# Optimization experiments

Measured on AMD Instinct MI355X. Metric: run time of the kernel, lower is better.

The kernel has to match this reference:

```python
import jax, jax.numpy as jnp
import numpy as np
from jax import lax

SIZE = 64
N_SUPPORT = 8192
N_QUERIES = 16384
UNROLLING_STEPS = 10


def setup_inputs() -> dict:
    key = jax.random.key(0)
    ks = jax.random.split(key, 6)
    s = 1.0 / np.sqrt(SIZE)
    return {
        "support": jax.random.normal(ks[0], (N_SUPPORT, SIZE), jnp.float32),
        "queries": jax.random.normal(ks[1], (N_QUERIES, SIZE), jnp.float32),
        "W_ih": jax.random.normal(ks[2], (4 * SIZE, SIZE), jnp.float32) * s,
        "W_hh": jax.random.normal(ks[3], (4 * SIZE, SIZE), jnp.float32) * s,
        "b_ih": jax.random.normal(ks[4], (4 * SIZE,), jnp.float32) * s,
        "b_hh": jax.random.normal(ks[5], (4 * SIZE,), jnp.float32) * s,
    }


def _lstm_cell(x, h, c, W_ih, W_hh, b_ih, b_hh):
    # PyTorch LSTMCell gate order: i, f, g, o
    gates = x @ W_ih.T + b_ih + h @ W_hh.T + b_hh  # [B, 4*size]
    i, f, g, o = jnp.split(gates, 4, axis=1)
    c_new = jax.nn.sigmoid(f) * c + jax.nn.sigmoid(i) * jnp.tanh(g)
    h_new = jax.nn.sigmoid(o) * jnp.tanh(c_new)
    return h_new, c_new


def reference(support, queries, W_ih, W_hh, b_ih, b_hh):
    def step(carry, _):
        h_hat, c = carry
        h = h_hat + queries                              # [B, size]
        att = jax.nn.softmax(h @ support.T, axis=1)      # [B, n_support]
        readout = att @ support                          # [B, size]
        h_hat2, c2 = _lstm_cell(queries, h + readout, c, W_ih, W_hh, b_ih, b_hh)
        return (h_hat2, c2), None

    init = (jnp.zeros_like(queries), jnp.zeros_like(queries))
    (h_hat, _), _ = lax.scan(step, init, None, length=UNROLLING_STEPS)
    return h_hat + queries
```

## Files before the change

kernel.cpp:

```cpp
#include <hip/hip_runtime.h>

using u16 = unsigned short;
using u32 = unsigned int;

#define NS 8192
#define NQ 16384
#define SZ 64
#define STEPS 10
#define TS 64
#define TSZ (TS * SZ)
#define NT (NS / TS)
#define NR (NT / 2)
#define L2E 1.44269504088896340736f

typedef __attribute__((ext_vector_type(8))) _Float16 f16x8;
typedef __attribute__((ext_vector_type(4))) float f32x4;

static __device__ __forceinline__ float ex2(float x) { float r; asm("v_exp_f32 %0, %1" : "=v"(r) : "v"(x)); return r; }
static __device__ __forceinline__ float rcp_(float x) { float r; asm("v_rcp_f32 %0, %1" : "=v"(r) : "v"(x)); return r; }

static __device__ __forceinline__ u16 hbits(_Float16 h) { union { _Float16 h; u16 u; } c; c.h = h; return c.u; }
static __device__ __forceinline__ u32 pk2(float lo, float hi) {
    return (u32)hbits((_Float16)lo) | ((u32)hbits((_Float16)hi) << 16);
}
static __device__ __forceinline__ f32x4 MMH(f16x8 a, f16x8 b, f32x4 c) {
    return __builtin_amdgcn_mfma_f32_16x16x32_f16(a, b, c, 0, 0, 0);
}
static __device__ __forceinline__ f16x8 LD(const void* p) { return *(const f16x8*)p; }
static __device__ __forceinline__ float sig(float x) { return rcp_(1.f + ex2(-L2E * x)); }
static __device__ __forceinline__ float tanh_(float x) {
    float e = ex2(-2.f * L2E * x);
    return (1.f - e) * rcp_(1.f + e);
}
static __device__ __forceinline__ void lds_fence() {
    asm volatile("s_waitcnt lgkmcnt(0)" ::: "memory");
    __builtin_amdgcn_sched_barrier(0);
}
static __device__ __forceinline__ void gload16(const void* g, void* l) {
    __builtin_amdgcn_global_load_lds(
        (const __attribute__((address_space(1))) void*)g,
        (__attribute__((address_space(3))) void*)l, 16, 0, 0);
}

__global__ void prep_kernel(const float* __restrict__ sup,
                            const float* __restrict__ Wih,
                            const float* __restrict__ Whh,
                            const float* __restrict__ bih,
                            const float* __restrict__ bhh,
                            u16* __restrict__ supH, u16* __restrict__ supL,
                            u16* __restrict__ supT,
                            u16* __restrict__ WiH, u16* __restrict__ WiL,
                            u16* __restrict__ WhH, u16* __restrict__ WhL,
                            float* __restrict__ bs) {
    int i = blockIdx.x * 256 + threadIdx.x;
    if (i < NS * SZ) {
        float v = sup[i];
        _Float16 hi = (_Float16)v;
        _Float16 lo = (_Float16)(v - (float)hi);
        supH[i] = hbits(hi);
        supL[i] = hbits(lo);
        int s = i >> 6, d = i & 63;
        supT[(s >> 6) * TSZ + d * TS + (s & 63)] = hbits(hi);
    }
    if (i < 4 * SZ * SZ) {
        float a = Wih[i]; _Float16 ah = (_Float16)a;
        WiH[i] = hbits(ah); WiL[i] = hbits((_Float16)(a - (float)ah));
        float b = Whh[i]; _Float16 bh = (_Float16)b;
        WhH[i] = hbits(bh); WhL[i] = hbits((_Float16)(b - (float)bh));
    }
    if (i < 4 * SZ) bs[i] = bih[i] + bhh[i];
}

__global__ __launch_bounds__(1024) void attlstm_kernel(
    const float* __restrict__ queries,
    const u16* __restrict__ supH, const u16* __restrict__ supL,
    const u16* __restrict__ supT,
    const u16* __restrict__ WiH, const u16* __restrict__ WiL,
    const u16* __restrict__ WhH, const u16* __restrict__ WhL,
    const float* __restrict__ bsum,
    float* __restrict__ out) {
    __shared__ __align__(16) u16 stage[4][3][TSZ];
    __shared__ __align__(16) u32 P_lds[16][512];
    __shared__ __align__(16) u16 hsl[4][2048];
    __shared__ __align__(16) float bs_lds[256];

    const int tid = threadIdx.x;
    const int w = tid >> 6;
    const int l = tid & 63;
    const int qg = w & 3;
    const int quarter = w >> 2;
    const int tsel = quarter >> 1;
    const int shalf = quarter & 1;
    const int q = l & 15;
    const int g = l >> 4;
    const int qrow = blockIdx.x * 64 + qg * 16 + q;
    const u32 swz = (u32)(q & 7) << 4;
    const u32 bsl = (u32)q * 128 + ((32u * (u32)quarter + 8u * (u32)g) ^ swz);

    if (tid < 256) bs_lds[tid] = bsum[tid];

    const u16* gsrc[3]; int inoff[3]; int ctsel[3];
#pragma unroll
    for (int j = 0; j < 3; ++j) {
        int c = w + 16 * j;
        ctsel[j] = c / 24;
        int rem = c - 24 * ctsel[j];
        int a = rem >> 3, s8 = rem & 7;
        int srcoff = (s8 * 8 + (l >> 3)) * SZ + ((l & 7) ^ (l >> 3)) * 8;
        gsrc[j] = ((a == 0) ? supH : (a == 1) ? supL : supT) + srcoff;
        inoff[j] = a * TSZ + s8 * 512;
    }
    u16* stg = &stage[0][0][0];
    char* hslb = (char*)&hsl[qg][0];
    char* pw = (char*)&P_lds[w][0];

    float qv[4], hh[4], cc[4];
    {
        f32x4 v = *(const f32x4*)&queries[qrow * SZ + 16 * quarter + 4 * g];
#pragma unroll
        for (int jj = 0; jj < 4; ++jj) { qv[jj] = v[jj]; hh[jj] = 0.f; cc[jj] = 0.f; }
        _Float16 c0 = (_Float16)v[0], c1 = (_Float16)v[1], c2 = (_Float16)v[2], c3 = (_Float16)v[3];
        uint2 whi, wlo;
        whi.x = (u32)hbits(c0) | ((u32)hbits(c1) << 16);
        whi.y = (u32)hbits(c2) | ((u32)hbits(c3) << 16);
        wlo.x = pk2(v[0] - (float)c0, v[1] - (float)c1);
        wlo.y = pk2(v[2] - (float)c2, v[3] - (float)c3);
        *(uint2*)(hslb + bsl) = whi;
        *(uint2*)(hslb + 2048 + bsl) = wlo;
    }
    __syncthreads();
    const f16x8 qfh0 = LD(hslb + q * 128 + ((16u * g) ^ swz));
    const f16x8 qfh1 = LD(hslb + q * 128 + ((16u * g + 64u) ^ swz));
    const f16x8 qfl0 = LD(hslb + 2048 + q * 128 + ((16u * g) ^ swz));
    const f16x8 qfl1 = LD(hslb + 2048 + q * 128 + ((16u * g + 64u) ^ swz));

#pragma unroll 1
    for (int step = 0; step < STEPS; ++step) {
        __syncthreads();
        {
            float h0 = hh[0] + qv[0], h1 = hh[1] + qv[1], h2 = hh[2] + qv[2], h3 = hh[3] + qv[3];
            _Float16 a0 = (_Float16)h0, a1 = (_Float16)h1, a2 = (_Float16)h2, a3 = (_Float16)h3;
            uint2 whi, wlo;
            whi.x = (u32)hbits(a0) | ((u32)hbits(a1) << 16);
            whi.y = (u32)hbits(a2) | ((u32)hbits(a3) << 16);
            wlo.x = pk2(h0 - (float)a0, h1 - (float)a1);
            wlo.y = pk2(h2 - (float)a2, h3 - (float)a3);
            *(uint2*)(hslb + bsl) = whi;
            *(uint2*)(hslb + 2048 + bsl) = wlo;
        }
        __syncthreads();
        const f16x8 bh0 = LD(hslb + q * 128 + ((16u * g) ^ swz));
        const f16x8 bh1 = LD(hslb + q * 128 + ((16u * g + 64u) ^ swz));
        const f16x8 bl0 = LD(hslb + 2048 + q * 128 + ((16u * g) ^ swz));
        const f16x8 bl1 = LD(hslb + 2048 + q * 128 + ((16u * g + 64u) ^ swz));

#pragma unroll
        for (int j = 0; j < 3; ++j)
            gload16(gsrc[j] + ctsel[j] * TSZ, stg + ctsel[j] * 12288 + inoff[j]);
        __syncthreads();

        float m = -1e30f, mL = -1.5e30f, lsum = 0.f;
        f32x4 Oa[4] = {{0, 0, 0, 0}, {0, 0, 0, 0}, {0, 0, 0, 0}, {0, 0, 0, 0}};

#pragma unroll 1
        for (int r = 0; r < NR; ++r) {
            if (r < NR - 1) {
#pragma unroll
                for (int j = 0; j < 3; ++j) {
                    int t = 2 * r + 2 + ctsel[j];
                    gload16(gsrc[j] + t * TSZ, stg + (t & 3) * 12288 + inoff[j]);
                }
            }
            const int myslot = (2 * r + tsel) & 3;
            const char* sH = (const char*)(stg + myslot * 12288);
            const char* sL = sH + TSZ * 2;
            const char* sT = sH + 2 * TSZ * 2;
            f32x4 sv[2];
#pragma unroll
            for (int sub = 0; sub < 2; ++sub) {
                u32 rb = (u32)(16 * (2 * shalf + sub) + q) * 128;
                f16x8 aH0 = LD(sH + rb + ((16u * g) ^ swz));
                f16x8 aH1 = LD(sH + rb + ((16u * g + 64u) ^ swz));
                f16x8 aL0 = LD(sL + rb + ((16u * g) ^ swz));
                f16x8 aL1 = LD(sL + rb + ((16u * g + 64u) ^ swz));
                f32x4 a = {0, 0, 0, 0};
                a = MMH(aH0, bh0, a); a = MMH(aH1, bh1, a);
                a = MMH(aH0, bl0, a); a = MMH(aH1, bl1, a);
                a = MMH(aL0, bh0, a); a = MMH(aL1, bh1, a);
                sv[sub] = a;
            }
            float tm = fmaxf(fmaxf(fmaxf(sv[0][0], sv[0][1]), fmaxf(sv[0][2], sv[0][3])),
                             fmaxf(fmaxf(sv[1][0], sv[1][1]), fmaxf(sv[1][2], sv[1][3])));
            tm = fmaxf(tm, __shfl_xor(tm, 16));
            tm = fmaxf(tm, __shfl_xor(tm, 32));
            if (__any(tm > m + 5.5f)) {
                float mn = fmaxf(m, tm);
                float sc = ex2((m - mn) * L2E);
                lsum *= sc;
                Oa[0] *= sc; Oa[1] *= sc; Oa[2] *= sc; Oa[3] *= sc;
                m = mn; mL = m * L2E;
            }
#pragma unroll
            for (int sub = 0; sub < 2; ++sub) {
                float p0 = ex2(sv[sub][0] * L2E - mL);
                float p1 = ex2(sv[sub][1] * L2E - mL);
                float p2 = ex2(sv[sub][2] * L2E - mL);
                float p3 = ex2(sv[sub][3] * L2E - mL);
                lsum += (p0 + p1) + (p2 + p3);
                uint2 wv; wv.x = pk2(p0, p1); wv.y = pk2(p2, p3);
                *(uint2*)(pw + q * 128 + ((32u * sub + 8u * g) ^ swz)) = wv;
            }
            lds_fence();
            f16x8 pb = LD(pw + q * 128 + ((16u * g) ^ swz));
            u32 kbT = (16u * g + 64u * shalf) ^ swz;
#pragma unroll
            for (int dsub = 0; dsub < 4; ++dsub) {
                f16x8 aT = LD(sT + (u32)(16 * dsub + q) * 128 + kbT);
                Oa[dsub] = MMH(aT, pb, Oa[dsub]);
            }
            __syncthreads();
        }
        lsum += __shfl_xor(lsum, 16);
        lsum += __shfl_xor(lsum, 32);

        float* mg = (float*)stg;
        float* mine = mg + (u32)(w * 64 + l) * 20;
        *(f32x4*)(mine + 0) = Oa[0];
        *(f32x4*)(mine + 4) = Oa[1];
        *(f32x4*)(mine + 8) = Oa[2];
        *(f32x4*)(mine + 12) = Oa[3];
        mine[16] = m; mine[17] = lsum;
        __syncthreads();

        float mk[4], lk[4];
        f32x4 Ok[4];
#pragma unroll
        for (int k = 0; k < 4; ++k) {
            const float* oth = mg + (u32)((qg + 4 * k) * 64 + l) * 20;
            Ok[k] = *(const f32x4*)(oth + 4 * quarter);
            mk[k] = oth[16]; lk[k] = oth[17];
        }
        float M = fmaxf(fmaxf(mk[0], mk[1]), fmaxf(mk[2], mk[3]));
        f32x4 Op = {0, 0, 0, 0};
        float ls = 0.f;
#pragma unroll
        for (int k = 0; k < 4; ++k) {
            float sk = ex2((mk[k] - M) * L2E);
            ls += lk[k] * sk;
            Op += Ok[k] * sk;
        }
        float inv = rcp_(ls);

        {
            float r0 = hh[0] + qv[0] + Op[0] * inv;
            float r1 = hh[1] + qv[1] + Op[1] * inv;
            float r2 = hh[2] + qv[2] + Op[2] * inv;
            float r3 = hh[3] + qv[3] + Op[3] * inv;
            _Float16 a0 = (_Float16)r0, a1 = (_Float16)r1, a2 = (_Float16)r2, a3 = (_Float16)r3;
            uint2 whi, wlo;
            whi.x = (u32)hbits(a0) | ((u32)hbits(a1) << 16);
            whi.y = (u32)hbits(a2) | ((u32)hbits(a3) << 16);
            wlo.x = pk2(r0 - (float)a0, r1 - (float)a1);
            wlo.y = pk2(r2 - (float)a2, r3 - (float)a3);
            *(uint2*)(hslb + bsl) = whi;
            *(uint2*)(hslb + 2048 + bsl) = wlo;
        }
        __syncthreads();
        const f16x8 rh0 = LD(hslb + q * 128 + ((16u * g) ^ swz));
        const f16x8 rh1 = LD(hslb + q * 128 + ((16u * g + 64u) ^ swz));
        const f16x8 rl0 = LD(hslb + 2048 + q * 128 + ((16u * g) ^ swz));
        const f16x8 rl1 = LD(hslb + 2048 + q * 128 + ((16u * g + 64u) ^ swz));

        f32x4 ga[4];
#pragma unroll
        for (int ch = 0; ch < 4; ++ch) {
            int u_ = 4 * ch + quarter;
            f32x4 a = *(const f32x4*)&bs_lds[16 * u_ + 4 * g];
            const u16* wiH = WiH + (16 * u_ + q) * SZ + 8 * g;
            const u16* wiL = WiL + (16 * u_ + q) * SZ + 8 * g;
            const u16* whH = WhH + (16 * u_ + q) * SZ + 8 * g;
            const u16* whL = WhL + (16 * u_ + q) * SZ + 8 * g;
            f16x8 w0 = LD(wiH), w1 = LD(wiH + 32);
            a = MMH(w0, qfh0, a); a = MMH(w1, qfh1, a);
            a = MMH(w0, qfl0, a); a = MMH(w1, qfl1, a);
            a = MMH(LD(wiL), qfh0, a); a = MMH(LD(wiL + 32), qfh1, a);
            f16x8 v0 = LD(whH), v1 = LD(whH + 32);
            a = MMH(v0, rh0, a); a = MMH(v1, rh1, a);
            a = MMH(v0, rl0, a); a = MMH(v1, rl1, a);
            a = MMH(LD(whL), rh0, a); a = MMH(LD(whL + 32), rh1, a);
            ga[ch] = a;
        }
#pragma unroll
        for (int jj = 0; jj < 4; ++jj) {
            float gi = sig(ga[0][jj]);
            float gf = sig(ga[1][jj]);
            float gg = tanh_(ga[2][jj]);
            float go = sig(ga[3][jj]);
            float cn = gf * cc[jj] + gi * gg;
            cc[jj] = cn;
            hh[jj] = go * tanh_(cn);
        }
    }

    {
        f32x4 v;
#pragma unroll
        for (int jj = 0; jj < 4; ++jj) v[jj] = hh[jj] + qv[jj];
        *(f32x4*)&out[qrow * SZ + 16 * quarter + 4 * g] = v;
    }
}

extern "C" void kernel_launch(void* const* d_in, const int* in_sizes, int n_in,
                              void* d_out, int out_size, void* d_ws, size_t ws_size,
                              hipStream_t stream) {
    const float* support = (const float*)d_in[0];
    const float* queries = (const float*)d_in[1];
    const float* W_ih = (const float*)d_in[2];
    const float* W_hh = (const float*)d_in[3];
    const float* b_ih = (const float*)d_in[4];
    const float* b_hh = (const float*)d_in[5];
    float* out = (float*)d_out;

    u16* supH = (u16*)d_ws;
    u16* supL = supH + NS * SZ;
    u16* supT = supL + NS * SZ;
    u16* WiH = supT + NS * SZ;
    u16* WiL = WiH + 4 * SZ * SZ;
    u16* WhH = WiL + 4 * SZ * SZ;
    u16* WhL = WhH + 4 * SZ * SZ;
    float* bs = (float*)(WhL + 4 * SZ * SZ);

    prep_kernel<<<(NS * SZ) / 256, 256, 0, stream>>>(support, W_ih, W_hh, b_ih, b_hh,
                                                     supH, supL, supT, WiH, WiL, WhH, WhL, bs);
    attlstm_kernel<<<NQ / 64, 1024, 0, stream>>>(queries, supH, supL, supT,
                                                 WiH, WiL, WhH, WhL, bs, out);
}
```

Before: 1.316 ms.

## Load transposed support directly into registers instead of staging through LDS

The transposed-support operand for the P·V MFMA is no longer staged through LDS via global_load_lds. Each wave now reads its four f16x8 fragments straight from global memory (L2) at the start of each round. This shrinks the LDS staging buffer by a third and cuts the per-round LDS traffic and LDS reads, at the cost of more scattered global loads whose latency must be hidden within the round. It also switches probability packing to the cvt_pkrtz instruction (round-toward-zero) and reorganises the cross-wave merge layout into strided f32x4 and float2 arrays.

After: 1.889 ms. 1.44x slower.

```diff
diff --git a/kernel.cpp b/kernel.cpp
--- a/kernel.cpp
+++ b/kernel.cpp
@@ -14,6 +14,7 @@
 #define L2E 1.44269504088896340736f
 
 typedef __attribute__((ext_vector_type(8))) _Float16 f16x8;
+typedef __attribute__((ext_vector_type(2))) __fp16 fp16x2;
 typedef __attribute__((ext_vector_type(4))) float f32x4;
 
 static __device__ __forceinline__ float ex2(float x) { float r; asm("v_exp_f32 %0, %1" : "=v"(r) : "v"(x)); return r; }
@@ -22,6 +23,10 @@
 static __device__ __forceinline__ u16 hbits(_Float16 h) { union { _Float16 h; u16 u; } c; c.h = h; return c.u; }
 static __device__ __forceinline__ u32 pk2(float lo, float hi) {
     return (u32)hbits((_Float16)lo) | ((u32)hbits((_Float16)hi) << 16);
+}
+static __device__ __forceinline__ u32 pkrtz(float a, float b) {
+    fp16x2 h = __builtin_amdgcn_cvt_pkrtz(a, b);
+    union { fp16x2 h; u32 u; } c; c.h = h; return c.u;
 }
 static __device__ __forceinline__ f32x4 MMH(f16x8 a, f16x8 b, f32x4 c) {
     return __builtin_amdgcn_mfma_f32_16x16x32_f16(a, b, c, 0, 0, 0);
@@ -79,7 +84,7 @@
     const u16* __restrict__ WhH, const u16* __restrict__ WhL,
     const float* __restrict__ bsum,
     float* __restrict__ out) {
-    __shared__ __align__(16) u16 stage[4][3][TSZ];
+    __shared__ __align__(16) u16 stage[4][2][TSZ];
     __shared__ __align__(16) u32 P_lds[16][512];
     __shared__ __align__(16) u16 hsl[4][2048];
     __shared__ __align__(16) float bs_lds[256];
@@ -99,20 +104,14 @@
 
     if (tid < 256) bs_lds[tid] = bsum[tid];
 
-    const u16* gsrc[3]; int inoff[3]; int ctsel[3];
-#pragma unroll
-    for (int j = 0; j < 3; ++j) {
-        int c = w + 16 * j;
-        ctsel[j] = c / 24;
-        int rem = c - 24 * ctsel[j];
-        int a = rem >> 3, s8 = rem & 7;
-        int srcoff = (s8 * 8 + (l >> 3)) * SZ + ((l & 7) ^ (l >> 3)) * 8;
-        gsrc[j] = ((a == 0) ? supH : (a == 1) ? supL : supT) + srcoff;
-        inoff[j] = a * TSZ + s8 * 512;
-    }
+    const int a_ = w >> 3, s8 = w & 7;
+    const int srcoff = (s8 * 8 + (l >> 3)) * SZ + ((l & 7) ^ (l >> 3)) * 8;
+    const u16* abase = (a_ == 0) ? supH : supL;
+    const int inoff = a_ * TSZ + s8 * 512;
     u16* stg = &stage[0][0][0];
     char* hslb = (char*)&hsl[qg][0];
     char* pw = (char*)&P_lds[w][0];
+    const u16* pTbase = supT + q * TS + 8 * g + 32 * shalf;
 
     float qv[4], hh[4], cc[4];
     {
@@ -154,9 +153,8 @@
         const f16x8 bl0 = LD(hslb + 2048 + q * 128 + ((16u * g) ^ swz));
         const f16x8 bl1 = LD(hslb + 2048 + q * 128 + ((16u * g + 64u) ^ swz));
 
-#pragma unroll
-        for (int j = 0; j < 3; ++j)
-            gload16(gsrc[j] + ctsel[j] * TSZ, stg + ctsel[j] * 12288 + inoff[j]);
+        gload16(abase + 0 * TSZ + srcoff, stg + 0 * (2 * TSZ) + inoff);
+        gload16(abase + 1 * TSZ + srcoff, stg + 1 * (2 * TSZ) + inoff);
         __syncthreads();
 
         float m = -1e30f, mL = -1.5e30f, lsum = 0.f;
@@ -164,17 +162,19 @@
 
 #pragma unroll 1
         for (int r = 0; r < NR; ++r) {
+            const int tme = 2 * r + tsel;
+            const u16* pT = pTbase + tme * TSZ;
+            f16x8 vT0 = LD(pT);
+            f16x8 vT1 = LD(pT + 16 * TS);
+            f16x8 vT2 = LD(pT + 32 * TS);
+            f16x8 vT3 = LD(pT + 48 * TS);
             if (r < NR - 1) {
-#pragma unroll
-                for (int j = 0; j < 3; ++j) {
-                    int t = 2 * r + 2 + ctsel[j];
-                    gload16(gsrc[j] + t * TSZ, stg + (t & 3) * 12288 + inoff[j]);
-                }
+                const int tA = 2 * r + 2, tB = 2 * r + 3;
+                gload16(abase + tA * TSZ + srcoff, stg + (tA & 3) * (2 * TSZ) + inoff);
+                gload16(abase + tB * TSZ + srcoff, stg + (tB & 3) * (2 * TSZ) + inoff);
             }
-            const int myslot = (2 * r + tsel) & 3;
-            const char* sH = (const char*)(stg + myslot * 12288);
+            const char* sH = (const char*)(stg + (tme & 3) * (2 * TSZ));
             const char* sL = sH + TSZ * 2;
-            const char* sT = sH + 2 * TSZ * 2;
             f32x4 sv[2];
 #pragma unroll
             for (int sub = 0; sub < 2; ++sub) {
@@ -207,38 +207,35 @@
                 float p2 = ex2(sv[sub][2] * L2E - mL);
                 float p3 = ex2(sv[sub][3] * L2E - mL);
                 lsum += (p0 + p1) + (p2 + p3);
-                uint2 wv; wv.x = pk2(p0, p1); wv.y = pk2(p2, p3);
+                uint2 wv; wv.x = pkrtz(p0, p1); wv.y = pkrtz(p2, p3);
                 *(uint2*)(pw + q * 128 + ((32u * sub + 8u * g) ^ swz)) = wv;
             }
             lds_fence();
             f16x8 pb = LD(pw + q * 128 + ((16u * g) ^ swz));
-            u32 kbT = (16u * g + 64u * shalf) ^ swz;
-#pragma unroll
-            for (int dsub = 0; dsub < 4; ++dsub) {
-                f16x8 aT = LD(sT + (u32)(16 * dsub + q) * 128 + kbT);
-                Oa[dsub] = MMH(aT, pb, Oa[dsub]);
-            }
+            Oa[0] = MMH(vT0, pb, Oa[0]);
+            Oa[1] = MMH(vT1, pb, Oa[1]);
+            Oa[2] = MMH(vT2, pb, Oa[2]);
+            Oa[3] = MMH(vT3, pb, Oa[3]);
             __syncthreads();
         }
         lsum += __shfl_xor(lsum, 16);
         lsum += __shfl_xor(lsum, 32);
 
-        float* mg = (float*)stg;
-        float* mine = mg + (u32)(w * 64 + l) * 20;
-        *(f32x4*)(mine + 0) = Oa[0];
-        *(f32x4*)(mine + 4) = Oa[1];
-        *(f32x4*)(mine + 8) = Oa[2];
-        *(f32x4*)(mine + 12) = Oa[3];
-        mine[16] = m; mine[17] = lsum;
+        f32x4* mg = (f32x4*)stg;
+        float2* ml = (float2*)&P_lds[0][0];
+#pragma unroll
+        for (int p = 0; p < 4; ++p)
+            mg[(u32)(((qg * 4 + quarter) * 4 + p) * 64 + l)] = Oa[p];
+        ml[(u32)((qg * 4 + quarter) * 64 + l)] = make_float2(m, lsum);
         __syncthreads();
 
         float mk[4], lk[4];
         f32x4 Ok[4];
 #pragma unroll
         for (int k = 0; k < 4; ++k) {
-            const float* oth = mg + (u32)((qg + 4 * k) * 64 + l) * 20;
-            Ok[k] = *(const f32x4*)(oth + 4 * quarter);
-            mk[k] = oth[16]; lk[k] = oth[17];
+            Ok[k] = mg[(u32)(((qg * 4 + k) * 4 + quarter) * 64 + l)];
+            float2 t = ml[(u32)((qg * 4 + k) * 64 + l)];
+            mk[k] = t.x; lk[k] = t.y;
         }
         float M = fmaxf(fmaxf(mk[0], mk[1]), fmaxf(mk[2], mk[3]));
         f32x4 Op = {0, 0, 0, 0};
```
